# Kernel tuning notes

Measured on AMD Instinct MI355X. Metric: run time of the kernel, lower is better.

Reference implementation:

```python
import jax, jax.numpy as jnp
import numpy as np

K = 12  # Emb.k: piece-type planes (6 types x 2 colors)
DOUT = 256
B = 16384          # number of positions (bags)
AVG_LEN = 30       # avg active features per position
T = B * AVG_LEN    # total ragged ids
S = (1.0 / 30.0) ** 0.5  # 1/sqrt(kRoughEstimateOfNumberOfOnesInInput)

# vertical board flip permutation over the 64 king squares
_SQ = np.arange(64)
_FLIP_PERM = jnp.asarray((7 - _SQ // 8) * 8 + _SQ % 8)


def _flip_vertical(x):
    # x: [64, K, 8, 8, d] -> flip ranks, swap color planes, flip king square
    x = jnp.flip(x, axis=2)
    x = jnp.roll(x, K // 2, axis=1)
    return x[_FLIP_PERM]


def setup_inputs() -> dict:
    key = jax.random.key(0)
    ks = jax.random.split(key, 8)
    pieces = jax.random.normal(ks[0], (64, K, 1, 1, DOUT), dtype=jnp.float32) * S
    ranks = jax.random.normal(ks[1], (64, K, 8, 1, DOUT), dtype=jnp.float32) * S
    files = jax.random.normal(ks[2], (64, K, 1, 8, DOUT), dtype=jnp.float32) * S
    tiles = jax.random.normal(ks[3], (64, K, 8, 8, DOUT), dtype=jnp.float32) * S
    mask = jnp.ones((64, K, 8, 8, 1), dtype=jnp.float32)
    mask = (mask.at[:, 0, 0, :, :].set(0.0)
                .at[:, 0, 7, :, :].set(0.0)
                .at[:, K // 2, 0, :, :].set(0.0)
                .at[:, K // 2, 7, :, :].set(0.0))
    # ragged lengths that sum exactly to T: antithetic pairs around AVG_LEN
    half = B // 2
    d = jax.random.randint(ks[4], (half,), -10, 11)
    lengths = jnp.concatenate([AVG_LEN + d, AVG_LEN - d]).astype(jnp.int64)
    values = jax.random.randint(ks[5], (T,), 0, K * 64).astype(jnp.int64)
    kings = jax.random.randint(ks[6], (B, 2), 0, 64).astype(jnp.int64)
    return dict(pieces=pieces, ranks=ranks, files=files, tiles=tiles,
                factorization_mask=mask, values=values, lengths=lengths, kings=kings)


def reference(pieces, ranks, files, tiles, factorization_mask, values, lengths, kings):
    # factorized merge: [64, K, 8, 8, d]
    merged = tiles + (pieces + ranks + files) * factorization_mask
    d = merged.shape[-1]
    w = merged.reshape(64 * K * 64, d)
    flipped = _flip_vertical(merged).reshape(64 * K * 64, d)

    n_bags = lengths.shape[0]
    total = values.shape[0]
    # segment id for each ragged element (== repeat_interleave of bag index)
    seg = jnp.repeat(jnp.arange(n_bags), lengths, total_repeat_length=total)
    piece_dim = K * 64
    mover_ids = kings[seg, 0] * piece_dim + values
    waiter_ids = kings[seg, 1] * piece_dim + values

    a = jax.ops.segment_sum(w[mover_ids], seg, num_segments=n_bags)
    b = jax.ops.segment_sum(flipped[waiter_ids], seg, num_segments=n_bags)
    return jnp.clip(a, 0.0, 1.0), jnp.clip(b, 0.0, 1.0)
```

## Files before the change

kernel.cpp:

```cpp
#include <hip/hip_runtime.h>

#define DOUT 256
#define NROWS 49152
#define SKS 768
#define MAT_BLOCKS SKS

__device__ __forceinline__ float4 ld4(const float* p) {
  return *reinterpret_cast<const float4*>(p);
}
__device__ __forceinline__ void acc4(float4& a, const float4 b) {
  a.x += b.x; a.y += b.y; a.z += b.z; a.w += b.w;
}

__global__ __launch_bounds__(256) void prep_kernel(
    const float* __restrict__ tiles, const float* __restrict__ pieces,
    const float* __restrict__ ranks, const float* __restrict__ files,
    const float* __restrict__ mask, float* __restrict__ merged,
    const int* __restrict__ lengths, const int* __restrict__ kings,
    int* __restrict__ offs, int* __restrict__ perm_m, int* __restrict__ perm_w,
    int n_bags) {
  const int bid = blockIdx.x;
  const int t = threadIdx.x;
  if (bid < MAT_BLOCKS) {
    const int sk = bid;
    const float pc = pieces[sk * 256 + t];
    float rk[8], fl[8];
#pragma unroll
    for (int r = 0; r < 8; ++r) rk[r] = ranks[(size_t)(sk * 8 + r) * 256 + t];
#pragma unroll
    for (int f = 0; f < 8; ++f) fl[f] = files[(size_t)(sk * 8 + f) * 256 + t];
    const float* trow = tiles + (size_t)sk * 64 * 256;
    float* orow = merged + (size_t)sk * 64 * 256;
    const float* mrow = mask + sk * 64;
#pragma unroll 4
    for (int p = 0; p < 64; ++p) {
      const float m = mrow[p];
      orow[p * 256 + t] = fmaf(pc + rk[p >> 3] + fl[p & 7], m, trow[p * 256 + t]);
    }
    return;
  }
  if (bid == MAT_BLOCKS) {
    __shared__ int part[256];
    const int chunk = (n_bags + 255) / 256;
    const int base = t * chunk;
    int s = 0;
    for (int j = 0; j < chunk; ++j) {
      int idx = base + j;
      if (idx < n_bags) s += lengths[idx];
    }
    part[t] = s;
    __syncthreads();
    for (int off = 1; off < 256; off <<= 1) {
      int v = (t >= off) ? part[t - off] : 0;
      __syncthreads();
      part[t] += v;
      __syncthreads();
    }
    int run = part[t] - s;
    for (int j = 0; j < chunk; ++j) {
      int idx = base + j;
      if (idx < n_bags) { offs[idx] = run; run += lengths[idx]; }
    }
    return;
  }
  const int col = bid - (MAT_BLOCKS + 1);
  int* __restrict__ perm = col ? perm_w : perm_m;
  __shared__ int hist[64];
  if (t < 64) hist[t] = 0;
  __syncthreads();
  for (int i = t; i < n_bags; i += 256) {
    atomicAdd(&hist[kings[2 * i + col]], 1);
  }
  __syncthreads();
  __shared__ int start[64];
  if (t == 0) {
    int run = 0;
    for (int k = 0; k < 64; ++k) { start[k] = run; run += hist[k]; }
  }
  __syncthreads();
  if (t < 64) hist[t] = start[t];
  __syncthreads();
  for (int i = t; i < n_bags; i += 256) {
    int pos = atomicAdd(&hist[kings[2 * i + col]], 1);
    perm[pos] = i;
  }
}

template <bool WAITER>
__device__ __forceinline__ void gather_body(
    const float* __restrict__ merged, const int* __restrict__ values,
    const int* __restrict__ lengths, const int* __restrict__ kings,
    const int* __restrict__ offs, const int* __restrict__ perm,
    float* __restrict__ out, int n_bags, int chunk, int b) {
  const int c = b & 7;
  const int j = b >> 3;
  const int pos = c * chunk + (j << 2) + (threadIdx.x >> 6);
  const int lim = min((c + 1) * chunk, n_bags);
  if (pos >= lim) return;
  const int lane = threadIdx.x & 63;
  const int bag = perm[pos];
  const int len = lengths[bag];
  const int kg = kings[2 * bag + (WAITER ? 1 : 0)];
  const int base = (WAITER ? (((7 - (kg >> 3)) << 3) + (kg & 7)) : kg) * 768;
  const int* __restrict__ vals = values + offs[bag];
  const float* __restrict__ mb = merged + (lane << 2);

  float4 a0 = {0.f, 0.f, 0.f, 0.f}, a1 = {0.f, 0.f, 0.f, 0.f};

  int i = 0;
  for (; i + 4 <= len; i += 4) {
    const int v0 = vals[i], v1 = vals[i + 1], v2 = vals[i + 2], v3 = vals[i + 3];
    unsigned r0, r1, r2, r3;
    if (WAITER) {
      const int k0 = v0 >> 6, k1 = v1 >> 6, k2 = v2 >> 6, k3 = v3 >> 6;
      r0 = base + ((k0 < 6 ? k0 + 6 : k0 - 6) << 6) + ((v0 & 63) ^ 56);
      r1 = base + ((k1 < 6 ? k1 + 6 : k1 - 6) << 6) + ((v1 & 63) ^ 56);
      r2 = base + ((k2 < 6 ? k2 + 6 : k2 - 6) << 6) + ((v2 & 63) ^ 56);
      r3 = base + ((k3 < 6 ? k3 + 6 : k3 - 6) << 6) + ((v3 & 63) ^ 56);
    } else {
      r0 = base + v0; r1 = base + v1; r2 = base + v2; r3 = base + v3;
    }
    const float4 x0 = ld4(mb + ((size_t)r0 << 8));
    const float4 x1 = ld4(mb + ((size_t)r1 << 8));
    const float4 x2 = ld4(mb + ((size_t)r2 << 8));
    const float4 x3 = ld4(mb + ((size_t)r3 << 8));
    acc4(a0, x0); acc4(a1, x1); acc4(a0, x2); acc4(a1, x3);
  }
  for (; i < len; ++i) {
    const int v = vals[i];
    unsigned r;
    if (WAITER) {
      const int k = v >> 6;
      r = base + ((k < 6 ? k + 6 : k - 6) << 6) + ((v & 63) ^ 56);
    } else {
      r = base + v;
    }
    acc4(a0, ld4(mb + ((size_t)r << 8)));
  }

  float4 o;
  o.x = fminf(fmaxf(a0.x + a1.x, 0.f), 1.f);
  o.y = fminf(fmaxf(a0.y + a1.y, 0.f), 1.f);
  o.z = fminf(fmaxf(a0.z + a1.z, 0.f), 1.f);
  o.w = fminf(fmaxf(a0.w + a1.w, 0.f), 1.f);
  float4* ob = reinterpret_cast<float4*>(out) +
               (WAITER ? (size_t)n_bags * 64 : 0);
  ob[(size_t)bag * 64 + lane] = o;
}

__global__ __launch_bounds__(256) void gather_kernel(
    const float* __restrict__ merged, const int* __restrict__ values,
    const int* __restrict__ lengths, const int* __restrict__ kings,
    const int* __restrict__ offs, const int* __restrict__ perm_m,
    const int* __restrict__ perm_w, float* __restrict__ out, int n_bags,
    int chunk, int half_blocks) {
  const int b = blockIdx.x;
  if (b < half_blocks) {
    gather_body<false>(merged, values, lengths, kings, offs, perm_m, out,
                       n_bags, chunk, b);
  } else {
    gather_body<true>(merged, values, lengths, kings, offs, perm_w, out,
                      n_bags, chunk, b - half_blocks);
  }
}

extern "C" void kernel_launch(void* const* d_in, const int* in_sizes, int n_in,
                              void* d_out, int out_size, void* d_ws, size_t ws_size,
                              hipStream_t stream) {
  const float* pieces = (const float*)d_in[0];
  const float* ranks  = (const float*)d_in[1];
  const float* files  = (const float*)d_in[2];
  const float* tiles  = (const float*)d_in[3];
  const float* mask   = (const float*)d_in[4];
  const int*   values = (const int*)d_in[5];
  const int*   lengths= (const int*)d_in[6];
  const int*   kings  = (const int*)d_in[7];
  float* out = (float*)d_out;

  const int B = in_sizes[6];

  const size_t bN = ((size_t)B * 4 + 255) & ~(size_t)255;
  int* offs   = (int*)d_ws;
  int* perm_m = (int*)((char*)d_ws + bN);
  int* perm_w = (int*)((char*)d_ws + 2 * bN);
  float* merged = (float*)((char*)d_ws + 3 * bN);

  prep_kernel<<<MAT_BLOCKS + 3, 256, 0, stream>>>(
      tiles, pieces, ranks, files, mask, merged, lengths, kings,
      offs, perm_m, perm_w, B);

  const int chunk = (B + 7) / 8;
  const int half_blocks = 8 * ((chunk + 3) / 4);
  gather_kernel<<<2 * half_blocks, 256, 0, stream>>>(
      merged, values, lengths, kings, offs, perm_m, perm_w, out, B,
      chunk, half_blocks);
}
```

Measured before the change: 206.5 us.

## Store merged table as bf16 and spread the merge across more blocks

The merged embedding table is now rounded to bf16 (round-to-nearest-even) and stored packed, so each gathered row is half the bytes; the gather widens bf16 to fp32 before accumulating. The prep merge is also reorganised so each block handles 4 rows with 64 lanes doing float4 loads, using 12288 blocks instead of 768. The aim is to halve gather bandwidth and write traffic and to increase parallelism in the merge. In exchange, the table values lose precision, which may push the output error past tolerance.

```diff
diff --git a/kernel.cpp b/kernel.cpp
--- a/kernel.cpp
+++ b/kernel.cpp
@@ -2,41 +2,56 @@
 
 #define DOUT 256
 #define NROWS 49152
-#define SKS 768
-#define MAT_BLOCKS SKS
+#define MAT_BLOCKS (NROWS / 4)
 
 __device__ __forceinline__ float4 ld4(const float* p) {
   return *reinterpret_cast<const float4*>(p);
 }
-__device__ __forceinline__ void acc4(float4& a, const float4 b) {
-  a.x += b.x; a.y += b.y; a.z += b.z; a.w += b.w;
+
+__device__ __forceinline__ unsigned rne2(float a, float b) {
+  unsigned ua = __float_as_uint(a), ub = __float_as_uint(b);
+  ua += 0x7FFFu + ((ua >> 16) & 1u);
+  ub += 0x7FFFu + ((ub >> 16) & 1u);
+  return (ua >> 16) | (ub & 0xFFFF0000u);
+}
+
+__device__ __forceinline__ void bf4_acc(uint2 w, float4& acc) {
+  acc.x += __uint_as_float(w.x << 16);
+  acc.y += __uint_as_float(w.x & 0xFFFF0000u);
+  acc.z += __uint_as_float(w.y << 16);
+  acc.w += __uint_as_float(w.y & 0xFFFF0000u);
 }
 
 __global__ __launch_bounds__(256) void prep_kernel(
     const float* __restrict__ tiles, const float* __restrict__ pieces,
     const float* __restrict__ ranks, const float* __restrict__ files,
-    const float* __restrict__ mask, float* __restrict__ merged,
+    const float* __restrict__ mask, uint2* __restrict__ merged,
     const int* __restrict__ lengths, const int* __restrict__ kings,
     int* __restrict__ offs, int* __restrict__ perm_m, int* __restrict__ perm_w,
     int n_bags) {
   const int bid = blockIdx.x;
   const int t = threadIdx.x;
   if (bid < MAT_BLOCKS) {
-    const int sk = bid;
-    const float pc = pieces[sk * 256 + t];
-    float rk[8], fl[8];
-#pragma unroll
-    for (int r = 0; r < 8; ++r) rk[r] = ranks[(size_t)(sk * 8 + r) * 256 + t];
-#pragma unroll
-    for (int f = 0; f < 8; ++f) fl[f] = files[(size_t)(sk * 8 + f) * 256 + t];
-    const float* trow = tiles + (size_t)sk * 64 * 256;
-    float* orow = merged + (size_t)sk * 64 * 256;
-    const float* mrow = mask + sk * 64;
-#pragma unroll 4
-    for (int p = 0; p < 64; ++p) {
-      const float m = mrow[p];
-      orow[p * 256 + t] = fmaf(pc + rk[p >> 3] + fl[p & 7], m, trow[p * 256 + t]);
-    }
+    const int row = (bid << 2) + (t >> 6);
+    const int lane = t & 63;
+    const int p = row & 63;
+    const int sk = row >> 6;
+    const int r = p >> 3, f = p & 7;
+    const float m = mask[row];
+    const int d0 = lane << 2;
+    float4 tl = ld4(tiles + (size_t)row * DOUT + d0);
+    float4 pc = ld4(pieces + (size_t)sk * DOUT + d0);
+    float4 rk = ld4(ranks + (size_t)(sk * 8 + r) * DOUT + d0);
+    float4 fl = ld4(files + (size_t)(sk * 8 + f) * DOUT + d0);
+    float4 o;
+    o.x = fmaf(pc.x + rk.x + fl.x, m, tl.x);
+    o.y = fmaf(pc.y + rk.y + fl.y, m, tl.y);
+    o.z = fmaf(pc.z + rk.z + fl.z, m, tl.z);
+    o.w = fmaf(pc.w + rk.w + fl.w, m, tl.w);
+    uint2 w;
+    w.x = rne2(o.x, o.y);
+    w.y = rne2(o.z, o.w);
+    merged[(size_t)row * 64 + lane] = w;
     return;
   }
   if (bid == MAT_BLOCKS) {
@@ -66,13 +81,13 @@
   const int col = bid - (MAT_BLOCKS + 1);
   int* __restrict__ perm = col ? perm_w : perm_m;
   __shared__ int hist[64];
+  __shared__ int start[64];
   if (t < 64) hist[t] = 0;
   __syncthreads();
   for (int i = t; i < n_bags; i += 256) {
     atomicAdd(&hist[kings[2 * i + col]], 1);
   }
   __syncthreads();
-  __shared__ int start[64];
   if (t == 0) {
     int run = 0;
     for (int k = 0; k < 64; ++k) { start[k] = run; run += hist[k]; }
@@ -88,7 +103,7 @@
 
 template <bool WAITER>
 __device__ __forceinline__ void gather_body(
-    const float* __restrict__ merged, const int* __restrict__ values,
+    const uint2* __restrict__ merged, const int* __restrict__ values,
     const int* __restrict__ lengths, const int* __restrict__ kings,
     const int* __restrict__ offs, const int* __restrict__ perm,
     float* __restrict__ out, int n_bags, int chunk, int b) {
@@ -103,7 +118,7 @@
   const int kg = kings[2 * bag + (WAITER ? 1 : 0)];
   const int base = (WAITER ? (((7 - (kg >> 3)) << 3) + (kg & 7)) : kg) * 768;
   const int* __restrict__ vals = values + offs[bag];
-  const float* __restrict__ mb = merged + (lane << 2);
+  const uint2* __restrict__ mb = merged + lane;
 
   float4 a0 = {0.f, 0.f, 0.f, 0.f}, a1 = {0.f, 0.f, 0.f, 0.f};
 
@@ -120,11 +135,11 @@
     } else {
       r0 = base + v0; r1 = base + v1; r2 = base + v2; r3 = base + v3;
     }
-    const float4 x0 = ld4(mb + ((size_t)r0 << 8));
-    const float4 x1 = ld4(mb + ((size_t)r1 << 8));
-    const float4 x2 = ld4(mb + ((size_t)r2 << 8));
-    const float4 x3 = ld4(mb + ((size_t)r3 << 8));
-    acc4(a0, x0); acc4(a1, x1); acc4(a0, x2); acc4(a1, x3);
+    const uint2 x0 = mb[(size_t)r0 << 6];
+    const uint2 x1 = mb[(size_t)r1 << 6];
+    const uint2 x2 = mb[(size_t)r2 << 6];
+    const uint2 x3 = mb[(size_t)r3 << 6];
+    bf4_acc(x0, a0); bf4_acc(x1, a1); bf4_acc(x2, a0); bf4_acc(x3, a1);
   }
   for (; i < len; ++i) {
     const int v = vals[i];
@@ -135,7 +150,7 @@
     } else {
       r = base + v;
     }
-    acc4(a0, ld4(mb + ((size_t)r << 8)));
+    bf4_acc(mb[(size_t)r << 6], a0);
   }
 
   float4 o;
@@ -149,7 +164,7 @@
 }
 
 __global__ __launch_bounds__(256) void gather_kernel(
-    const float* __restrict__ merged, const int* __restrict__ values,
+    const uint2* __restrict__ merged, const int* __restrict__ values,
     const int* __restrict__ lengths, const int* __restrict__ kings,
     const int* __restrict__ offs, const int* __restrict__ perm_m,
     const int* __restrict__ perm_w, float* __restrict__ out, int n_bags,
@@ -183,7 +198,7 @@
   int* offs   = (int*)d_ws;
   int* perm_m = (int*)((char*)d_ws + bN);
   int* perm_w = (int*)((char*)d_ws + 2 * bN);
-  float* merged = (float*)((char*)d_ws + 3 * bN);
+  uint2* merged = (uint2*)((char*)d_ws + 3 * bN);
 
   prep_kernel<<<MAT_BLOCKS + 3, 256, 0, stream>>>(
       tiles, pieces, ranks, files, mask, merged, lengths, kings,
```

Result: faster. 197.9 us (-4.2%).
